# Kernel optimization log

Measured on AMD Instinct MI355X. Metric: run time of the kernel, lower is better.

Reference implementation:

```python
import jax, jax.numpy as jnp
import numpy as np


def _ragged_reverse(x, lengths):
    # x: [N, L, C]; flip the first `lengths[n]` steps of each sample, zero-fill the rest.
    N, L, C = x.shape
    t = jnp.arange(L, dtype=lengths.dtype)[None, :]          # [1, L]
    Ln = lengths[:, None]                                     # [N, 1]
    valid = t < Ln                                            # [N, L]
    idx = jnp.where(valid, Ln - 1 - t, 0)                     # [N, L]
    rev = jnp.take_along_axis(x, idx[:, :, None], axis=1)     # [N, L, C]
    return jnp.where(valid[:, :, None], rev, jnp.zeros((), x.dtype))


def _gru(xb, W_ih, W_hh, b_ih, b_hh):
    # xb: [B, L, C] -> outputs [B, L, H] (standard torch GRU cell math).
    B, L, C = xb.shape
    H = W_hh.shape[0]
    xw = xb @ W_ih + b_ih                                     # [B, L, 3H], input proj done once

    def step(h, xw_t):
        gh = h @ W_hh + b_hh                                  # [B, 3H]
        xr, xz, xn = jnp.split(xw_t, 3, axis=-1)
        hr, hz, hn = jnp.split(gh, 3, axis=-1)
        r = jax.nn.sigmoid(xr + hr)
        z = jax.nn.sigmoid(xz + hz)
        n = jnp.tanh(xn + r * hn)
        h_new = (1.0 - z) * n + z * h
        return h_new, h_new

    h0 = jnp.zeros((B, H), xb.dtype)
    _, ys = jax.lax.scan(step, h0, jnp.swapaxes(xw, 0, 1))    # ys: [L, B, H]
    return jnp.swapaxes(ys, 0, 1)                             # [B, L, H]


def reference(x, lengths, W_ih, W_hh, b_ih, b_hh):
    N, L, C = x.shape
    # to_bidirection: stack [forward; ragged-reversed] along batch -> [2N, L, C]
    rev = _ragged_reverse(x, lengths)
    xb = jnp.concatenate([x, rev], axis=0)
    out = _gru(xb, W_ih, W_hh, b_ih, b_hh)                    # [2N, L, H]
    # from_bidirection: split halves, concat on feature dim -> [N, L, 2H]
    return jnp.concatenate([out[:N], out[N:]], axis=2)


def setup_inputs() -> dict:
    key = jax.random.key(0)
    ks = jax.random.split(key, 6)
    N, L, C, H = 32, 2048, 64, 128
    s = 1.0 / np.sqrt(H)
    return {
        "x": jax.random.normal(ks[0], (N, L, C), dtype=jnp.float32),
        "lengths": jax.random.randint(ks[1], (N,), 1, L + 1, dtype=jnp.int32),
        "W_ih": jax.random.normal(ks[2], (C, 3 * H), dtype=jnp.float32) * s,
        "W_hh": jax.random.normal(ks[3], (H, 3 * H), dtype=jnp.float32) * s,
        "b_ih": jax.random.normal(ks[4], (3 * H,), dtype=jnp.float32) * s,
        "b_hh": jax.random.normal(ks[5], (3 * H,), dtype=jnp.float32) * s,
    }
```

## Files before the change

### kernel.cpp

```cpp
#include <hip/hip_runtime.h>

#define L_SEQ 2048
#define C_IN  64
#define HH    128
#define NSEQ  32
#define B2    64
#define G3    384
#define RING  16
#define XW32  (C_IN / 2)
#define XTOT  (NSEQ * L_SEQ * XW32)

typedef _Float16 half2_t __attribute__((ext_vector_type(2)));

#define PINU(v) asm volatile("" : "+v"(v))
#define STEP_BARRIER() asm volatile("s_waitcnt lgkmcnt(0)\n\ts_barrier" ::: "memory")

__device__ __forceinline__ float fdot2u(unsigned int a, unsigned int b, float c) {
    return __builtin_amdgcn_fdot2(__builtin_bit_cast(half2_t, a),
                                  __builtin_bit_cast(half2_t, b), c, false);
}

__device__ __forceinline__ unsigned int pack_h2(float a, float b) {
    half2_t t; t.x = (_Float16)a; t.y = (_Float16)b;
    return __builtin_bit_cast(unsigned int, t);
}

__device__ __forceinline__ float qadd1(float x) {
    int t = __builtin_amdgcn_update_dpp(0, __builtin_bit_cast(int, x),
                                        0xB1, 0xF, 0xF, true);
    return x + __builtin_bit_cast(float, t);
}

__device__ __forceinline__ float fast_sigmoid(float x) {
    float e = __builtin_amdgcn_exp2f(-1.4426950408889634f * x);
    return __builtin_amdgcn_rcpf(1.0f + e);
}

__device__ __forceinline__ float fast_tanh(float x) {
    float a = fabsf(x);
    float e = __builtin_amdgcn_exp2f(-2.8853900817779268f * a);
    float r = (1.0f - e) * __builtin_amdgcn_rcpf(1.0f + e);
    return copysignf(r, x);
}

__device__ __forceinline__ float pdot32(const unsigned int (&w)[32],
                                        const unsigned int* __restrict__ xrow,
                                        float acc) {
    const uint4* x4 = (const uint4*)xrow;
#pragma unroll
    for (int i = 0; i < 8; ++i) {
        const uint4 v = x4[i];
        acc = fdot2u(v.x, w[4*i+0], acc);
        acc = fdot2u(v.y, w[4*i+1], acc);
        acc = fdot2u(v.z, w[4*i+2], acc);
        acc = fdot2u(v.w, w[4*i+3], acc);
    }
    return acc;
}

__global__ __launch_bounds__(256)
void pack_x_kernel(const float* __restrict__ x, unsigned int* __restrict__ xh)
{
    const size_t i = (size_t)blockIdx.x * 256 + threadIdx.x;
    if (i < (size_t)XTOT) {
        const float2 v = ((const float2*)x)[i];
        xh[i] = pack_h2(v.x, v.y);
    }
    if (i < XW32) xh[(size_t)XTOT + i] = 0u;
}

__global__ __launch_bounds__(512) __attribute__((amdgpu_waves_per_eu(1, 1)))
void bigru_fused(const unsigned int* __restrict__ xh,
                 const int* __restrict__ lengths,
                 const float* __restrict__ W_ih, const float* __restrict__ W_hh,
                 const float* __restrict__ b_ih, const float* __restrict__ b_hh,
                 float* __restrict__ out)
{
    __shared__ unsigned int hbufu[2][64];
    __shared__ float        ring[RING][G3];

    const int tid = threadIdx.x;
    const int s   = blockIdx.x;
    const bool isFwd = (s < NSEQ);
    const int  len   = isFwd ? L_SEQ : lengths[s - NSEQ];
    const unsigned int* __restrict__ xseq = xh + (size_t)(s % NSEQ) * L_SEQ * XW32;
    const unsigned int* __restrict__ zrow = xh + (size_t)XTOT;

    const bool consumer = (tid < 256);
    const int u = tid & 255;
    const int j = u >> 1;
    const int p = u & 1;

    unsigned int w0[32], w1[32], w2[32];
    float bA = 0.f, bB = 0.f;

    if (consumer) {
        const float* Wb = W_hh + (size_t)(64 * p) * G3;
#pragma unroll
        for (int k = 0; k < 32; ++k) {
            w0[k] = pack_h2(Wb[(2*k) * G3 + j],       Wb[(2*k+1) * G3 + j]);
            w1[k] = pack_h2(Wb[(2*k) * G3 + 128 + j], Wb[(2*k+1) * G3 + 128 + j]);
            w2[k] = pack_h2(Wb[(2*k) * G3 + 256 + j], Wb[(2*k+1) * G3 + 256 + j]);
        }
#pragma unroll
        for (int k = 0; k < 32; ++k) { PINU(w0[k]); PINU(w1[k]); PINU(w2[k]); }
        bA = b_hh[256 + j];
        if (tid < 64) hbufu[0][tid] = 0u;
    } else {
#pragma unroll
        for (int k = 0; k < 32; ++k)
            w0[k] = pack_h2(W_ih[(2*k) * G3 + u], W_ih[(2*k+1) * G3 + u]);
        bA = b_ih[u] + b_hh[u];
        if (u >= 128) {
            const int c1 = 128 + u;
#pragma unroll
            for (int k = 0; k < 32; ++k)
                w1[k] = pack_h2(W_ih[(2*k) * G3 + c1], W_ih[(2*k+1) * G3 + c1]);
            bB = b_ih[c1];
        }
#pragma unroll
        for (int k = 0; k < 32; ++k) { PINU(w0[k]); PINU(w1[k]); }

        for (int rd = 0; rd < 6; ++rd) {
            const int srcL = isFwd ? rd : (len - 1 - rd);
            const unsigned int* xrow =
                (srcL >= 0) ? (xseq + (size_t)srcL * XW32) : zrow;
            ring[rd][u] = pdot32(w0, xrow, bA);
            if (u >= 128) ring[rd][128 + u] = pdot32(w1, xrow, bB);
        }
    }
    __syncthreads();

    float cr = 0.f, cz = 0.f, cn = 0.f, hreg = 0.f;
    if (consumer) { cr = ring[0][j]; cz = ring[0][128 + j]; cn = ring[0][256 + j]; }

    float* outbase = out + (size_t)(s % NSEQ) * L_SEQ * 256 + (isFwd ? 0 : HH);
    int cur = 0;

    for (int t = 0; t < L_SEQ; ++t) {
        if (consumer) {
            const int sln = (t + 1) & (RING - 1);
            const float nr = ring[sln][j];
            const float nz = ring[sln][128 + j];
            const float nn = ring[sln][256 + j];
            float ar = 0.f, az = 0.f, an = 0.f;
            const uint4* hb = (const uint4*)&hbufu[cur][p * 32];
#pragma unroll
            for (int i = 0; i < 8; ++i) {
                const uint4 hv = hb[i];
                ar = fdot2u(hv.x, w0[4*i+0], ar); ar = fdot2u(hv.y, w0[4*i+1], ar);
                ar = fdot2u(hv.z, w0[4*i+2], ar); ar = fdot2u(hv.w, w0[4*i+3], ar);
                az = fdot2u(hv.x, w1[4*i+0], az); az = fdot2u(hv.y, w1[4*i+1], az);
                az = fdot2u(hv.z, w1[4*i+2], az); az = fdot2u(hv.w, w1[4*i+3], az);
                an = fdot2u(hv.x, w2[4*i+0], an); an = fdot2u(hv.y, w2[4*i+1], an);
                an = fdot2u(hv.z, w2[4*i+2], an); an = fdot2u(hv.w, w2[4*i+3], an);
            }
            ar = qadd1(ar); az = qadd1(az); an = qadd1(an);
            const float r = fast_sigmoid(cr + ar);
            const float z = fast_sigmoid(cz + az);
            const float n = fast_tanh(cn + r * (an + bA));
            const float hnew = z * (hreg - n) + n;
            hreg = hnew;
            if (p == 0) {
                ((_Float16*)&hbufu[cur ^ 1][0])[j] = (_Float16)hnew;
                outbase[(size_t)t * 256 + j] = hnew;
            }
            cur ^= 1;
            cr = nr; cz = nz; cn = nn;
        } else {
            const int rd = t + 6;
            if (rd < L_SEQ) {
                const int srcL = isFwd ? rd : (len - 1 - rd);
                const unsigned int* xrow =
                    (srcL >= 0) ? (xseq + (size_t)srcL * XW32) : zrow;
                const int sl = rd & (RING - 1);
                ring[sl][u] = pdot32(w0, xrow, bA);
                if (u >= 128) ring[sl][128 + u] = pdot32(w1, xrow, bB);
            }
        }
        STEP_BARRIER();
    }
}

extern "C" void kernel_launch(void* const* d_in, const int* in_sizes, int n_in,
                              void* d_out, int out_size, void* d_ws, size_t ws_size,
                              hipStream_t stream) {
    const float* x       = (const float*)d_in[0];
    const int*   lengths = (const int*)  d_in[1];
    const float* W_ih    = (const float*)d_in[2];
    const float* W_hh    = (const float*)d_in[3];
    const float* b_ih    = (const float*)d_in[4];
    const float* b_hh    = (const float*)d_in[5];
    float* out = (float*)d_out;

    unsigned int* xh = (unsigned int*)d_ws;

    pack_x_kernel<<<dim3((XTOT + 255) / 256), dim3(256), 0, stream>>>(x, xh);
    bigru_fused<<<dim3(B2), dim3(512), 0, stream>>>(
        xh, lengths, W_ih, W_hh, b_ih, b_hh, out);
}
```

Measured before the change: 1.149 ms.

## Batch 16 sequences per block and compute GRU steps with MFMA

Replaces the per-sequence producer/consumer dot-product kernel with a 4-block kernel in which each block processes 16 sequences together. Each step runs the recurrent and input projections as 16x16x32 f16 MFMA tiles, with the input term fused into the same accumulation instead of a precomputed ring buffer. This raises arithmetic efficiency per step, but only 4 CUs are used, so the 2048-step serial chain now rests on MFMA latency plus one barrier per step for 16 sequences at once. The output stores are also more scattered.

```diff
diff --git a/kernel.cpp b/kernel.cpp
--- a/kernel.cpp
+++ b/kernel.cpp
@@ -4,58 +4,34 @@
 #define C_IN  64
 #define HH    128
 #define NSEQ  32
-#define B2    64
 #define G3    384
-#define RING  16
 #define XW32  (C_IN / 2)
 #define XTOT  (NSEQ * L_SEQ * XW32)
-
+#define ROWH  136
+
+typedef _Float16 f16x8 __attribute__((ext_vector_type(8)));
+typedef float    f32x4 __attribute__((ext_vector_type(4)));
 typedef _Float16 half2_t __attribute__((ext_vector_type(2)));
 
-#define PINU(v) asm volatile("" : "+v"(v))
 #define STEP_BARRIER() asm volatile("s_waitcnt lgkmcnt(0)\n\ts_barrier" ::: "memory")
-
-__device__ __forceinline__ float fdot2u(unsigned int a, unsigned int b, float c) {
-    return __builtin_amdgcn_fdot2(__builtin_bit_cast(half2_t, a),
-                                  __builtin_bit_cast(half2_t, b), c, false);
-}
+#define MFMA16(a, b, c) __builtin_amdgcn_mfma_f32_16x16x32_f16((a), (b), (c), 0, 0, 0)
 
 __device__ __forceinline__ unsigned int pack_h2(float a, float b) {
     half2_t t; t.x = (_Float16)a; t.y = (_Float16)b;
     return __builtin_bit_cast(unsigned int, t);
 }
-
-__device__ __forceinline__ float qadd1(float x) {
-    int t = __builtin_amdgcn_update_dpp(0, __builtin_bit_cast(int, x),
-                                        0xB1, 0xF, 0xF, true);
-    return x + __builtin_bit_cast(float, t);
-}
-
+__device__ __forceinline__ f16x8 ld_frag_g(const unsigned int* p) {
+    return __builtin_bit_cast(f16x8, *(const uint4*)p);
+}
 __device__ __forceinline__ float fast_sigmoid(float x) {
     float e = __builtin_amdgcn_exp2f(-1.4426950408889634f * x);
     return __builtin_amdgcn_rcpf(1.0f + e);
 }
-
 __device__ __forceinline__ float fast_tanh(float x) {
     float a = fabsf(x);
     float e = __builtin_amdgcn_exp2f(-2.8853900817779268f * a);
     float r = (1.0f - e) * __builtin_amdgcn_rcpf(1.0f + e);
     return copysignf(r, x);
-}
-
-__device__ __forceinline__ float pdot32(const unsigned int (&w)[32],
-                                        const unsigned int* __restrict__ xrow,
-                                        float acc) {
-    const uint4* x4 = (const uint4*)xrow;
-#pragma unroll
-    for (int i = 0; i < 8; ++i) {
-        const uint4 v = x4[i];
-        acc = fdot2u(v.x, w[4*i+0], acc);
-        acc = fdot2u(v.y, w[4*i+1], acc);
-        acc = fdot2u(v.z, w[4*i+2], acc);
-        acc = fdot2u(v.w, w[4*i+3], acc);
-    }
-    return acc;
 }
 
 __global__ __launch_bounds__(256)
@@ -69,116 +45,164 @@
     if (i < XW32) xh[(size_t)XTOT + i] = 0u;
 }
 
-__global__ __launch_bounds__(512) __attribute__((amdgpu_waves_per_eu(1, 1)))
-void bigru_fused(const unsigned int* __restrict__ xh,
-                 const int* __restrict__ lengths,
-                 const float* __restrict__ W_ih, const float* __restrict__ W_hh,
-                 const float* __restrict__ b_ih, const float* __restrict__ b_hh,
-                 float* __restrict__ out)
+__global__ __launch_bounds__(256) __attribute__((amdgpu_waves_per_eu(1, 1)))
+void bigru_mfma(const unsigned int* __restrict__ xh, const int* __restrict__ lengths,
+                const float* __restrict__ W_ih, const float* __restrict__ W_hh,
+                const float* __restrict__ b_ih, const float* __restrict__ b_hh,
+                float* __restrict__ out)
 {
-    __shared__ unsigned int hbufu[2][64];
-    __shared__ float        ring[RING][G3];
+    __shared__ _Float16 hlds[2][16][ROWH];
 
     const int tid = threadIdx.x;
-    const int s   = blockIdx.x;
-    const bool isFwd = (s < NSEQ);
-    const int  len   = isFwd ? L_SEQ : lengths[s - NSEQ];
-    const unsigned int* __restrict__ xseq = xh + (size_t)(s % NSEQ) * L_SEQ * XW32;
-    const unsigned int* __restrict__ zrow = xh + (size_t)XTOT;
-
-    const bool consumer = (tid < 256);
-    const int u = tid & 255;
-    const int j = u >> 1;
-    const int p = u & 1;
-
-    unsigned int w0[32], w1[32], w2[32];
-    float bA = 0.f, bB = 0.f;
-
-    if (consumer) {
-        const float* Wb = W_hh + (size_t)(64 * p) * G3;
-#pragma unroll
-        for (int k = 0; k < 32; ++k) {
-            w0[k] = pack_h2(Wb[(2*k) * G3 + j],       Wb[(2*k+1) * G3 + j]);
-            w1[k] = pack_h2(Wb[(2*k) * G3 + 128 + j], Wb[(2*k+1) * G3 + 128 + j]);
-            w2[k] = pack_h2(Wb[(2*k) * G3 + 256 + j], Wb[(2*k+1) * G3 + 256 + j]);
-        }
-#pragma unroll
-        for (int k = 0; k < 32; ++k) { PINU(w0[k]); PINU(w1[k]); PINU(w2[k]); }
-        bA = b_hh[256 + j];
-        if (tid < 64) hbufu[0][tid] = 0u;
-    } else {
-#pragma unroll
-        for (int k = 0; k < 32; ++k)
-            w0[k] = pack_h2(W_ih[(2*k) * G3 + u], W_ih[(2*k+1) * G3 + u]);
-        bA = b_ih[u] + b_hh[u];
-        if (u >= 128) {
-            const int c1 = 128 + u;
-#pragma unroll
-            for (int k = 0; k < 32; ++k)
-                w1[k] = pack_h2(W_ih[(2*k) * G3 + c1], W_ih[(2*k+1) * G3 + c1]);
-            bB = b_ih[c1];
-        }
-#pragma unroll
-        for (int k = 0; k < 32; ++k) { PINU(w0[k]); PINU(w1[k]); }
-
-        for (int rd = 0; rd < 6; ++rd) {
-            const int srcL = isFwd ? rd : (len - 1 - rd);
-            const unsigned int* xrow =
-                (srcL >= 0) ? (xseq + (size_t)srcL * XW32) : zrow;
-            ring[rd][u] = pdot32(w0, xrow, bA);
-            if (u >= 128) ring[rd][128 + u] = pdot32(w1, xrow, bB);
-        }
+    const int w   = tid >> 6;
+    const int l   = tid & 63;
+    const int lm  = l & 15;
+    const int lg  = l >> 4;
+    const int blk = blockIdx.x;
+    const bool fwd = (blk < 2);
+
+    f16x8 Br[2][6], Bz[2][6], Bhn[2][4], Bxn[2][2];
+#pragma unroll
+    for (int e = 0; e < 2; ++e) {
+        const int col = 32*w + 16*e + lm;
+#pragma unroll
+        for (int kt = 0; kt < 6; ++kt) {
+            f16x8 fr, fz;
+#pragma unroll
+            for (int i = 0; i < 8; ++i) {
+                const int k = kt*32 + lg*8 + i;
+                const float vr = (k < HH) ? W_hh[k*G3 + col]
+                                          : W_ih[(k-HH)*G3 + col];
+                const float vz = (k < HH) ? W_hh[k*G3 + 128 + col]
+                                          : W_ih[(k-HH)*G3 + 128 + col];
+                fr[i] = (_Float16)vr; fz[i] = (_Float16)vz;
+            }
+            Br[e][kt] = fr; Bz[e][kt] = fz;
+        }
+#pragma unroll
+        for (int kt = 0; kt < 4; ++kt) {
+            f16x8 f;
+#pragma unroll
+            for (int i = 0; i < 8; ++i)
+                f[i] = (_Float16)W_hh[(kt*32 + lg*8 + i)*G3 + 256 + col];
+            Bhn[e][kt] = f;
+        }
+#pragma unroll
+        for (int kt = 0; kt < 2; ++kt) {
+            f16x8 f;
+#pragma unroll
+            for (int i = 0; i < 8; ++i)
+                f[i] = (_Float16)W_ih[(kt*32 + lg*8 + i)*G3 + 256 + col];
+            Bxn[e][kt] = f;
+        }
+    }
+    float biasR[2], biasZ[2], biasHN[2], biasXN[2];
+#pragma unroll
+    for (int e = 0; e < 2; ++e) {
+        const int col = 32*w + 16*e + lm;
+        biasR[e]  = b_ih[col] + b_hh[col];
+        biasZ[e]  = b_ih[128 + col] + b_hh[128 + col];
+        biasHN[e] = b_hh[256 + col];
+        biasXN[e] = b_ih[256 + col];
+    }
+
+    const int sA = 16*(blk & 1) + lm;
+    const unsigned int* __restrict__ xbase = xh + (size_t)sA * L_SEQ * XW32;
+    const unsigned int* __restrict__ zrow  = xh + (size_t)XTOT;
+    const int lenA = fwd ? 0 : lengths[sA];
+
+    auto xrow = [&](int t) -> const unsigned int* {
+        const int src = fwd ? t : (lenA - 1 - t);
+        return ((unsigned)src < (unsigned)L_SEQ) ? (xbase + (size_t)src * XW32)
+                                                 : zrow;
+    };
+
+    size_t obrow[4];
+#pragma unroll
+    for (int q = 0; q < 4; ++q)
+        obrow[q] = (size_t)(16*(blk & 1) + lg*4 + q) * L_SEQ * 256;
+    int colp[2];
+#pragma unroll
+    for (int e = 0; e < 2; ++e) colp[e] = 32*w + 16*e + lm + (fwd ? 0 : HH);
+
+    f32x4 ho0 = {0.f, 0.f, 0.f, 0.f}, ho1 = {0.f, 0.f, 0.f, 0.f};
+    {
+        unsigned int* hz = (unsigned int*)&hlds[0][0][0];
+        for (int i = tid; i < (int)(sizeof(hlds) / 4); i += 256) hz[i] = 0u;
     }
     __syncthreads();
 
-    float cr = 0.f, cz = 0.f, cn = 0.f, hreg = 0.f;
-    if (consumer) { cr = ring[0][j]; cz = ring[0][128 + j]; cn = ring[0][256 + j]; }
-
-    float* outbase = out + (size_t)(s % NSEQ) * L_SEQ * 256 + (isFwd ? 0 : HH);
+    f16x8 Ax0, Ax1;
+    { const unsigned int* p = xrow(0);
+      Ax0 = ld_frag_g(p + lg*4); Ax1 = ld_frag_g(p + 16 + lg*4); }
+
     int cur = 0;
-
     for (int t = 0; t < L_SEQ; ++t) {
-        if (consumer) {
-            const int sln = (t + 1) & (RING - 1);
-            const float nr = ring[sln][j];
-            const float nz = ring[sln][128 + j];
-            const float nn = ring[sln][256 + j];
-            float ar = 0.f, az = 0.f, an = 0.f;
-            const uint4* hb = (const uint4*)&hbufu[cur][p * 32];
-#pragma unroll
-            for (int i = 0; i < 8; ++i) {
-                const uint4 hv = hb[i];
-                ar = fdot2u(hv.x, w0[4*i+0], ar); ar = fdot2u(hv.y, w0[4*i+1], ar);
-                ar = fdot2u(hv.z, w0[4*i+2], ar); ar = fdot2u(hv.w, w0[4*i+3], ar);
-                az = fdot2u(hv.x, w1[4*i+0], az); az = fdot2u(hv.y, w1[4*i+1], az);
-                az = fdot2u(hv.z, w1[4*i+2], az); az = fdot2u(hv.w, w1[4*i+3], az);
-                an = fdot2u(hv.x, w2[4*i+0], an); an = fdot2u(hv.y, w2[4*i+1], an);
-                an = fdot2u(hv.z, w2[4*i+2], an); an = fdot2u(hv.w, w2[4*i+3], an);
+        const char* hp = (const char*)&hlds[cur][0][0] + lm*(2*ROWH) + lg*16;
+        const f16x8 Ah0 = __builtin_bit_cast(f16x8, *(const uint4*)(hp +   0));
+        const f16x8 Ah1 = __builtin_bit_cast(f16x8, *(const uint4*)(hp +  64));
+        const f16x8 Ah2 = __builtin_bit_cast(f16x8, *(const uint4*)(hp + 128));
+        const f16x8 Ah3 = __builtin_bit_cast(f16x8, *(const uint4*)(hp + 192));
+
+        f16x8 AxN0, AxN1;
+        { const unsigned int* p = xrow(t + 1);
+          AxN0 = ld_frag_g(p + lg*4); AxN1 = ld_frag_g(p + 16 + lg*4); }
+
+        _Float16* hnext = &hlds[cur ^ 1][0][0];
+
+        {
+            f32x4 cr = {biasR[0], biasR[0], biasR[0], biasR[0]};
+            cr = MFMA16(Ah0, Br[0][0], cr); cr = MFMA16(Ah1, Br[0][1], cr);
+            cr = MFMA16(Ah2, Br[0][2], cr); cr = MFMA16(Ah3, Br[0][3], cr);
+            cr = MFMA16(Ax0, Br[0][4], cr); cr = MFMA16(Ax1, Br[0][5], cr);
+            f32x4 cz = {biasZ[0], biasZ[0], biasZ[0], biasZ[0]};
+            cz = MFMA16(Ah0, Bz[0][0], cz); cz = MFMA16(Ah1, Bz[0][1], cz);
+            cz = MFMA16(Ah2, Bz[0][2], cz); cz = MFMA16(Ah3, Bz[0][3], cz);
+            cz = MFMA16(Ax0, Bz[0][4], cz); cz = MFMA16(Ax1, Bz[0][5], cz);
+            f32x4 chn = {biasHN[0], biasHN[0], biasHN[0], biasHN[0]};
+            chn = MFMA16(Ah0, Bhn[0][0], chn); chn = MFMA16(Ah1, Bhn[0][1], chn);
+            chn = MFMA16(Ah2, Bhn[0][2], chn); chn = MFMA16(Ah3, Bhn[0][3], chn);
+            f32x4 cxn = {biasXN[0], biasXN[0], biasXN[0], biasXN[0]};
+            cxn = MFMA16(Ax0, Bxn[0][0], cxn); cxn = MFMA16(Ax1, Bxn[0][1], cxn);
+#pragma unroll
+            for (int q = 0; q < 4; ++q) {
+                const float r = fast_sigmoid(cr[q]);
+                const float z = fast_sigmoid(cz[q]);
+                const float n = fast_tanh(cxn[q] + r * chn[q]);
+                const float h = z * (ho0[q] - n) + n;
+                ho0[q] = h;
+                hnext[(lg*4 + q) * ROWH + (32*w + lm)] = (_Float16)h;
+                out[obrow[q] + (size_t)t * 256 + colp[0]] = h;
             }
-            ar = qadd1(ar); az = qadd1(az); an = qadd1(an);
-            const float r = fast_sigmoid(cr + ar);
-            const float z = fast_sigmoid(cz + az);
-            const float n = fast_tanh(cn + r * (an + bA));
-            const float hnew = z * (hreg - n) + n;
-            hreg = hnew;
-            if (p == 0) {
-                ((_Float16*)&hbufu[cur ^ 1][0])[j] = (_Float16)hnew;
-                outbase[(size_t)t * 256 + j] = hnew;
+        }
+        {
+            f32x4 cr = {biasR[1], biasR[1], biasR[1], biasR[1]};
+            cr = MFMA16(Ah0, Br[1][0], cr); cr = MFMA16(Ah1, Br[1][1], cr);
+            cr = MFMA16(Ah2, Br[1][2], cr); cr = MFMA16(Ah3, Br[1][3], cr);
+            cr = MFMA16(Ax0, Br[1][4], cr); cr = MFMA16(Ax1, Br[1][5], cr);
+            f32x4 cz = {biasZ[1], biasZ[1], biasZ[1], biasZ[1]};
+            cz = MFMA16(Ah0, Bz[1][0], cz); cz = MFMA16(Ah1, Bz[1][1], cz);
+            cz = MFMA16(Ah2, Bz[1][2], cz); cz = MFMA16(Ah3, Bz[1][3], cz);
+            cz = MFMA16(Ax0, Bz[1][4], cz); cz = MFMA16(Ax1, Bz[1][5], cz);
+            f32x4 chn = {biasHN[1], biasHN[1], biasHN[1], biasHN[1]};
+            chn = MFMA16(Ah0, Bhn[1][0], chn); chn = MFMA16(Ah1, Bhn[1][1], chn);
+            chn = MFMA16(Ah2, Bhn[1][2], chn); chn = MFMA16(Ah3, Bhn[1][3], chn);
+            f32x4 cxn = {biasXN[1], biasXN[1], biasXN[1], biasXN[1]};
+            cxn = MFMA16(Ax0, Bxn[1][0], cxn); cxn = MFMA16(Ax1, Bxn[1][1], cxn);
+#pragma unroll
+            for (int q = 0; q < 4; ++q) {
+                const float r = fast_sigmoid(cr[q]);
+                const float z = fast_sigmoid(cz[q]);
+                const float n = fast_tanh(cxn[q] + r * chn[q]);
+                const float h = z * (ho1[q] - n) + n;
+                ho1[q] = h;
+                hnext[(lg*4 + q) * ROWH + (32*w + 16 + lm)] = (_Float16)h;
+                out[obrow[q] + (size_t)t * 256 + colp[1]] = h;
             }
-            cur ^= 1;
-            cr = nr; cz = nz; cn = nn;
-        } else {
-            const int rd = t + 6;
-            if (rd < L_SEQ) {
-                const int srcL = isFwd ? rd : (len - 1 - rd);
-                const unsigned int* xrow =
-                    (srcL >= 0) ? (xseq + (size_t)srcL * XW32) : zrow;
-                const int sl = rd & (RING - 1);
-                ring[sl][u] = pdot32(w0, xrow, bA);
-                if (u >= 128) ring[sl][128 + u] = pdot32(w1, xrow, bB);
-            }
         }
         STEP_BARRIER();
+        cur ^= 1;
+        Ax0 = AxN0; Ax1 = AxN1;
     }
 }
 
@@ -196,6 +220,6 @@
     unsigned int* xh = (unsigned int*)d_ws;
 
     pack_x_kernel<<<dim3((XTOT + 255) / 256), dim3(256), 0, stream>>>(x, xh);
-    bigru_fused<<<dim3(B2), dim3(512), 0, stream>>>(
+    bigru_mfma<<<dim3(4), dim3(256), 0, stream>>>(
         xh, lengths, W_ih, W_hh, b_ih, b_hh, out);
 }
```

Measured after the change: 1.713 ms. 49.1% more time.
